# Performance work log

Hardware: AMD Instinct MI355X
Metric: run time of the kernel (lower is better)

Reference implementation:

```python
import jax, jax.numpy as jnp
import numpy as np

B, N, DIM, H, DH = 8, 1024, 512, 8, 64
INNER = H * DH
SCALE = DH ** -0.5
EPS = 1e-12  # F.normalize eps


def setup_inputs() -> dict:
    key = jax.random.key(0)
    k1, k2, k3, k4, k5 = jax.random.split(key, 5)
    x = jax.random.normal(k1, (B, N, DIM), dtype=jnp.float32)
    spd = jax.random.normal(k2, (B, 1, N, N), dtype=jnp.float32)
    # per-head binomial keep mask (one realized draw of the original loop), guaranteed nonzero
    a = np.random.RandomState(0).binomial(1, 0.9, size=H)
    if a.sum() == 0:
        a[0] = 1
    head_mask = jnp.asarray(a, dtype=jnp.float32)
    W_qkv = jax.random.normal(k3, (DIM, 3 * INNER), dtype=jnp.float32) * (DIM ** -0.5)
    W_out = jax.random.normal(k4, (INNER, DIM), dtype=jnp.float32) * (INNER ** -0.5)
    b_out = jax.random.normal(k5, (DIM,), dtype=jnp.float32) * 0.01
    return {"x": x, "spd": spd, "head_mask": head_mask,
            "W_qkv": W_qkv, "W_out": W_out, "b_out": b_out}


def reference(x, spd, head_mask, W_qkv, W_out, b_out):
    b, n, _ = x.shape
    qkv = x @ W_qkv                                   # [b, n, 3*inner]
    q, k, v = jnp.split(qkv, 3, axis=-1)
    split_heads = lambda t: t.reshape(b, n, H, DH).transpose(0, 2, 1, 3)  # b h n d
    q, k, v = split_heads(q), split_heads(k), split_heads(v)

    dots = jnp.einsum('bhnd,bhmd->bhnm', q, k) * SCALE        # [b,h,n,n]
    prod = dots * spd                                         # broadcast spd over heads
    prod_norm = jnp.sqrt(jnp.sum(prod * prod, axis=-1, keepdims=True))
    dots_norm = jnp.sqrt(jnp.sum(dots * dots, axis=-1, keepdims=True))
    bias = prod / jnp.maximum(prod_norm, EPS) * dots_norm     # F.normalize(prod)*||dots||
    attn = jax.nn.softmax(dots + bias, axis=-1)

    # head dropout mask with rescale: attn * mask * H / sum(mask)
    scale_m = head_mask * (H / jnp.sum(head_mask))
    attn = attn * scale_m[None, :, None, None]

    out = jnp.einsum('bhnm,bhmd->bhnd', attn, v)              # [b,h,n,d]
    out = out.transpose(0, 2, 1, 3).reshape(b, n, INNER)      # b n (h d)
    return out @ W_out + b_out
```

## Files before the change

### kernel.cpp

```cpp
#include <hip/hip_runtime.h>
#include <hip/hip_bf16.h>

typedef __attribute__((ext_vector_type(8))) short short8;
typedef __attribute__((ext_vector_type(4))) short s16x4;
typedef __attribute__((ext_vector_type(4))) float f32x4;

typedef const __attribute__((address_space(1))) unsigned* gp1;
typedef __attribute__((address_space(3))) unsigned* lp3;

__device__ inline short f2bf(float f) {
    union { float f; unsigned u; } v; v.f = f;
    unsigned r = v.u + 0x7fffu + ((v.u >> 16) & 1u);
    return (short)(r >> 16);
}

__global__ __launch_bounds__(256) void cvt_bf16(
    const float* __restrict__ src, short* __restrict__ dst, int n4)
{
    int i = blockIdx.x * 256 + threadIdx.x;
    if (i < n4) {
        float4 v = ((const float4*)src)[i];
        s16x4 o = { f2bf(v.x), f2bf(v.y), f2bf(v.z), f2bf(v.w) };
        ((s16x4*)dst)[i] = o;
    }
}

__global__ __launch_bounds__(256) void tr_w(
    const float* __restrict__ src, short* __restrict__ dst, int K, int N)
{
    __shared__ float t[64][65];
    const int k0 = blockIdx.x * 64, n0 = blockIdx.y * 64;
    const int r = threadIdx.x >> 4, c4 = (threadIdx.x & 15) * 4;
#pragma unroll
    for (int j = 0; j < 4; j++) {
        float4 v = *(const float4*)(src + (size_t)(k0 + r + 16 * j) * N + n0 + c4);
        t[r + 16 * j][c4 + 0] = v.x; t[r + 16 * j][c4 + 1] = v.y;
        t[r + 16 * j][c4 + 2] = v.z; t[r + 16 * j][c4 + 3] = v.w;
    }
    __syncthreads();
#pragma unroll
    for (int j = 0; j < 4; j++) {
        const int n = r + 16 * j;
        s16x4 o = { f2bf(t[c4 + 0][n]), f2bf(t[c4 + 1][n]),
                    f2bf(t[c4 + 2][n]), f2bf(t[c4 + 3][n]) };
        *(s16x4*)(dst + (size_t)(n0 + n) * K + k0 + c4) = o;
    }
}

__global__ __launch_bounds__(256) void qkv_gemm(
    const short* __restrict__ A, const short* __restrict__ BT,
    short* __restrict__ q, short* __restrict__ k, short* __restrict__ vt)
{
    __shared__ short sA[128][32];
    __shared__ short sB[64][32];

    const int tid  = threadIdx.x;
    const int wv   = tid >> 6, lane = tid & 63;
    const int quad = lane >> 4, l16 = lane & 15;
    const int m0 = blockIdx.x * 128, n0 = blockIdx.y * 64;

    f32x4 acc[2][4];
#pragma unroll
    for (int i = 0; i < 2; i++)
#pragma unroll
        for (int j = 0; j < 4; j++) acc[i][j] = (f32x4){0.f, 0.f, 0.f, 0.f};

    const short* a_src = A  + (size_t)(m0 + wv * 32 + (lane >> 2)) * 512 + (lane & 3) * 8;
    const short* b_src = BT + (size_t)(n0 + wv * 16 + (lane >> 2)) * 512 + (lane & 3) * 8;
    char* a_dst = (char*)sA + wv * 2048;
    char* b_dst = (char*)sB + wv * 1024;

    for (int ks = 0; ks < 16; ks++) {
        __syncthreads();
        const short* ap = a_src + ks * 32;
        const short* bp = b_src + ks * 32;
        __builtin_amdgcn_global_load_lds((gp1)(ap),            (lp3)(a_dst),        16, 0, 0);
        __builtin_amdgcn_global_load_lds((gp1)(ap + 16 * 512), (lp3)(a_dst + 1024), 16, 0, 0);
        __builtin_amdgcn_global_load_lds((gp1)(bp),            (lp3)(b_dst),        16, 0, 0);
        __syncthreads();

        short8 af[2], bf[4];
#pragma unroll
        for (int f = 0; f < 2; f++)
            af[f] = *(const short8*)&sA[wv * 32 + f * 16 + l16][quad * 8];
#pragma unroll
        for (int f = 0; f < 4; f++)
            bf[f] = *(const short8*)&sB[f * 16 + l16][quad * 8];
#pragma unroll
        for (int fm = 0; fm < 2; fm++)
#pragma unroll
            for (int fn = 0; fn < 4; fn++)
                acc[fm][fn] = __builtin_amdgcn_mfma_f32_16x16x32_bf16(
                    af[fm], bf[fn], acc[fm][fn], 0, 0, 0);
    }

    const int sec = n0 >> 9;
#pragma unroll
    for (int fn = 0; fn < 4; fn++) {
        const int gc = n0 + fn * 16 + l16;
        const int cc = gc & 511;
        const int h = cc >> 6, d = cc & 63;
#pragma unroll
        for (int fm = 0; fm < 2; fm++)
#pragma unroll
            for (int i = 0; i < 4; i++) {
                const int gm = m0 + wv * 32 + fm * 16 + quad * 4 + i;
                const int b = gm >> 10, n = gm & 1023;
                const int bh = b * 8 + h;
                if (sec == 0)      q[((size_t)(bh * 1024 + n)) * 64 + d] = f2bf(acc[fm][fn][i] * 0.125f);
                else if (sec == 1) k[((size_t)(bh * 1024 + n)) * 64 + d] = f2bf(acc[fm][fn][i]);
                else               vt[((size_t)(bh * 64 + d)) * 1024 + n] = f2bf(acc[fm][fn][i]);
            }
    }
}

__global__ __launch_bounds__(256, 4) void attn_k(
    const short* __restrict__ q, const short* __restrict__ kk,
    const short* __restrict__ vt, const float* __restrict__ spd,
    const float* __restrict__ hm, short* __restrict__ o)
{
    __shared__ short sK[64][72];
    __shared__ short sV[64][72];
    __shared__ short sP[4][16][72];
    __shared__ float sred[4][16];

    const int tid  = threadIdx.x;
    const int wv   = tid >> 6, lane = tid & 63;
    const int quad = lane >> 4, l16 = lane & 15;
    const int qt = blockIdx.x, bh = blockIdx.y;
    const int b = bh >> 3, h = bh & 7;
    const int q0 = qt * 64;

    const short* qb = q + ((size_t)bh * 1024 + q0 + wv * 16 + l16) * 64;
    short8 aq0 = *(const short8*)(qb + quad * 8);
    short8 aq1 = *(const short8*)(qb + 32 + quad * 8);

    const int sr = tid & 31, sc = (tid >> 5) * 8;
    const short* ksrc = kk + (size_t)bh * 65536 + (size_t)sr * 64 + sc;
    const short* vsrc = vt + (size_t)bh * 65536 + (size_t)sr * 1024 + sc;
    const float* sp   = spd + ((size_t)b * 1024 + q0 + wv * 16 + l16) * 1024 + quad * 4;

    float dn = 0.f, pn = 0.f, mxs = -1e30f, mxp = -1e30f;
    short8 k0 = *(const short8*)(ksrc);
    short8 k1 = *(const short8*)(ksrc + 2048);
    float4 sv0 = *(const float4*)(sp +  0);
    float4 sv1 = *(const float4*)(sp + 16);
    float4 sv2 = *(const float4*)(sp + 32);
    float4 sv3 = *(const float4*)(sp + 48);

    for (int c = 0; c < 16; ++c) {
        __syncthreads();
        *(short8*)&sK[sr][sc]      = k0;
        *(short8*)&sK[sr + 32][sc] = k1;
        __syncthreads();
        float4 svc0 = sv0, svc1 = sv1, svc2 = sv2, svc3 = sv3;
        if (c < 15) {
            k0 = *(const short8*)(ksrc + (c + 1) * 4096);
            k1 = *(const short8*)(ksrc + (c + 1) * 4096 + 2048);
            sv0 = *(const float4*)(sp + (c + 1) * 64 +  0);
            sv1 = *(const float4*)(sp + (c + 1) * 64 + 16);
            sv2 = *(const float4*)(sp + (c + 1) * 64 + 32);
            sv3 = *(const float4*)(sp + (c + 1) * 64 + 48);
        }
        f32x4 a[4];
#pragma unroll
        for (int t = 0; t < 4; t++) {
            a[t] = (f32x4){0.f, 0.f, 0.f, 0.f};
            a[t] = __builtin_amdgcn_mfma_f32_16x16x32_bf16(
                *(const short8*)&sK[t * 16 + l16][quad * 8], aq0, a[t], 0, 0, 0);
            a[t] = __builtin_amdgcn_mfma_f32_16x16x32_bf16(
                *(const short8*)&sK[t * 16 + l16][32 + quad * 8], aq1, a[t], 0, 0, 0);
        }
        const float4 svv[4] = {svc0, svc1, svc2, svc3};
#pragma unroll
        for (int t = 0; t < 4; t++)
#pragma unroll
            for (int i = 0; i < 4; i++) {
                float s  = a[t][i];
                float sv = ((const float*)&svv[t])[i];
                float ps = s * sv;
                dn = fmaf(s, s, dn);
                pn = fmaf(ps, ps, pn);
                mxs = fmaxf(mxs, s);
                mxp = fmaxf(mxp, ps);
            }
    }
    dn  += __shfl_xor(dn, 16, 64);  dn  += __shfl_xor(dn, 32, 64);
    pn  += __shfl_xor(pn, 16, 64);  pn  += __shfl_xor(pn, 32, 64);
    mxs = fmaxf(mxs, __shfl_xor(mxs, 16, 64)); mxs = fmaxf(mxs, __shfl_xor(mxs, 32, 64));
    mxp = fmaxf(mxp, __shfl_xor(mxp, 16, 64)); mxp = fmaxf(mxp, __shfl_xor(mxp, 32, 64));
    const float ratio = sqrtf(dn) / fmaxf(sqrtf(pn), 1e-12f);
    const float Mhat  = mxs + ratio * mxp;

    float ls = 0.f;
    f32x4 O[4];
#pragma unroll
    for (int dt = 0; dt < 4; dt++) O[dt] = (f32x4){0.f, 0.f, 0.f, 0.f};

    k0 = *(const short8*)(ksrc);
    k1 = *(const short8*)(ksrc + 2048);
    short8 v0 = *(const short8*)(vsrc);
    short8 v1 = *(const short8*)(vsrc + 32768);

    for (int c = 0; c < 16; ++c) {
        __syncthreads();
        *(short8*)&sK[sr][sc]      = k0;
        *(short8*)&sK[sr + 32][sc] = k1;
        *(short8*)&sV[sr][sc]      = v0;
        *(short8*)&sV[sr + 32][sc] = v1;
        __syncthreads();
        float4 svc0 = *(const float4*)(sp + c * 64 +  0);
        float4 svc1 = *(const float4*)(sp + c * 64 + 16);
        float4 svc2 = *(const float4*)(sp + c * 64 + 32);
        float4 svc3 = *(const float4*)(sp + c * 64 + 48);
        if (c < 15) {
            k0 = *(const short8*)(ksrc + (c + 1) * 4096);
            k1 = *(const short8*)(ksrc + (c + 1) * 4096 + 2048);
            v0 = *(const short8*)(vsrc + (c + 1) * 64);
            v1 = *(const short8*)(vsrc + (c + 1) * 64 + 32768);
        }
        f32x4 a[4];
#pragma unroll
        for (int t = 0; t < 4; t++) {
            a[t] = (f32x4){0.f, 0.f, 0.f, 0.f};
            a[t] = __builtin_amdgcn_mfma_f32_16x16x32_bf16(
                *(const short8*)&sK[t * 16 + l16][quad * 8], aq0, a[t], 0, 0, 0);
            a[t] = __builtin_amdgcn_mfma_f32_16x16x32_bf16(
                *(const short8*)&sK[t * 16 + l16][32 + quad * 8], aq1, a[t], 0, 0, 0);
        }
        const float4 svv[4] = {svc0, svc1, svc2, svc3};
#pragma unroll
        for (int t = 0; t < 4; t++) {
            float p0, p1, p2, p3;
            {
                float s = a[t][0], sv = ((const float*)&svv[t])[0];
                p0 = __expf(s * fmaf(sv, ratio, 1.0f) - Mhat);
            }
            {
                float s = a[t][1], sv = ((const float*)&svv[t])[1];
                p1 = __expf(s * fmaf(sv, ratio, 1.0f) - Mhat);
            }
            {
                float s = a[t][2], sv = ((const float*)&svv[t])[2];
                p2 = __expf(s * fmaf(sv, ratio, 1.0f) - Mhat);
            }
            {
                float s = a[t][3], sv = ((const float*)&svv[t])[3];
                p3 = __expf(s * fmaf(sv, ratio, 1.0f) - Mhat);
            }
            ls += (p0 + p1) + (p2 + p3);
            s16x4 pk = { f2bf(p0), f2bf(p1), f2bf(p2), f2bf(p3) };
            *(s16x4*)&sP[wv][l16][t * 16 + quad * 4] = pk;
        }
#pragma unroll
        for (int kc = 0; kc < 2; kc++) {
            short8 pa = *(const short8*)&sP[wv][l16][kc * 32 + quad * 8];
#pragma unroll
            for (int dt = 0; dt < 4; dt++) {
                short8 vf = *(const short8*)&sV[dt * 16 + l16][kc * 32 + quad * 8];
                O[dt] = __builtin_amdgcn_mfma_f32_16x16x32_bf16(pa, vf, O[dt], 0, 0, 0);
            }
        }
    }
    ls += __shfl_xor(ls, 16, 64); ls += __shfl_xor(ls, 32, 64);
    const float hsum = hm[0] + hm[1] + hm[2] + hm[3] + hm[4] + hm[5] + hm[6] + hm[7];
    const float rinv = hm[h] * 8.0f / (hsum * ls);
    if (quad == 0) sred[wv][l16] = rinv;
    __syncthreads();
    float rv[4];
#pragma unroll
    for (int i = 0; i < 4; i++) rv[i] = sred[wv][quad * 4 + i];
#pragma unroll
    for (int dt = 0; dt < 4; dt++)
#pragma unroll
        for (int i = 0; i < 4; i++)
            o[((size_t)(b * 1024 + q0 + wv * 16 + quad * 4 + i)) * 512 + h * 64 + dt * 16 + l16]
                = f2bf(O[dt][i] * rv[i]);
}

__global__ __launch_bounds__(256) void out_gemm(
    const short* __restrict__ A, const short* __restrict__ BT,
    const float* __restrict__ bias, float* __restrict__ out)
{
    __shared__ short sA[128][32];
    __shared__ short sB[64][32];

    const int tid  = threadIdx.x;
    const int wv   = tid >> 6, lane = tid & 63;
    const int quad = lane >> 4, l16 = lane & 15;
    const int m0 = blockIdx.x * 128, n0 = blockIdx.y * 64;

    f32x4 acc[2][4];
#pragma unroll
    for (int i = 0; i < 2; i++)
#pragma unroll
        for (int j = 0; j < 4; j++) acc[i][j] = (f32x4){0.f, 0.f, 0.f, 0.f};

    const short* a_src = A  + (size_t)(m0 + wv * 32 + (lane >> 2)) * 512 + (lane & 3) * 8;
    const short* b_src = BT + (size_t)(n0 + wv * 16 + (lane >> 2)) * 512 + (lane & 3) * 8;
    char* a_dst = (char*)sA + wv * 2048;
    char* b_dst = (char*)sB + wv * 1024;

    for (int ks = 0; ks < 16; ks++) {
        __syncthreads();
        const short* ap = a_src + ks * 32;
        const short* bp = b_src + ks * 32;
        __builtin_amdgcn_global_load_lds((gp1)(ap),            (lp3)(a_dst),        16, 0, 0);
        __builtin_amdgcn_global_load_lds((gp1)(ap + 16 * 512), (lp3)(a_dst + 1024), 16, 0, 0);
        __builtin_amdgcn_global_load_lds((gp1)(bp),            (lp3)(b_dst),        16, 0, 0);
        __syncthreads();

        short8 af[2], bf[4];
#pragma unroll
        for (int f = 0; f < 2; f++)
            af[f] = *(const short8*)&sA[wv * 32 + f * 16 + l16][quad * 8];
#pragma unroll
        for (int f = 0; f < 4; f++)
            bf[f] = *(const short8*)&sB[f * 16 + l16][quad * 8];
#pragma unroll
        for (int fm = 0; fm < 2; fm++)
#pragma unroll
            for (int fn = 0; fn < 4; fn++)
                acc[fm][fn] = __builtin_amdgcn_mfma_f32_16x16x32_bf16(
                    af[fm], bf[fn], acc[fm][fn], 0, 0, 0);
    }

#pragma unroll
    for (int fn = 0; fn < 4; fn++) {
        const int gc = n0 + fn * 16 + l16;
        const float bv = bias[gc];
#pragma unroll
        for (int fm = 0; fm < 2; fm++)
#pragma unroll
            for (int i = 0; i < 4; i++) {
                const int gm = m0 + wv * 32 + fm * 16 + quad * 4 + i;
                out[(size_t)gm * 512 + gc] = acc[fm][fn][i] + bv;
            }
    }
}

extern "C" void kernel_launch(void* const* d_in, const int* in_sizes, int n_in,
                              void* d_out, int out_size, void* d_ws, size_t ws_size,
                              hipStream_t stream) {
    const float* x    = (const float*)d_in[0];
    const float* spd  = (const float*)d_in[1];
    const float* hm   = (const float*)d_in[2];
    const float* Wqkv = (const float*)d_in[3];
    const float* Wout = (const float*)d_in[4];
    const float* bout = (const float*)d_in[5];
    float* out = (float*)d_out;

    char* ws = (char*)d_ws;
    short* qw  = (short*)(ws);
    short* kw  = (short*)(ws + ((size_t)8  << 20));
    short* vtw = (short*)(ws + ((size_t)16 << 20));
    short* ow  = (short*)(ws + ((size_t)24 << 20));
    short* xb  = (short*)(ws + ((size_t)32 << 20));
    short* wqT = (short*)(ws + ((size_t)40 << 20));
    short* woT = (short*)(ws + ((size_t)42 << 20));

    cvt_bf16<<<4096, 256, 0, stream>>>(x, xb, 8192 * 512 / 4);
    tr_w    <<<dim3(8, 24), 256, 0, stream>>>(Wqkv, wqT, 512, 1536);
    tr_w    <<<dim3(8, 8),  256, 0, stream>>>(Wout, woT, 512, 512);

    qkv_gemm<<<dim3(64, 24), 256, 0, stream>>>(xb, wqT, qw, kw, vtw);
    attn_k  <<<dim3(16, 64), 256, 0, stream>>>(qw, kw, vtw, spd, hm, ow);
    out_gemm<<<dim3(64, 8),  256, 0, stream>>>(ow, woT, bout, out);
}
```

Measured before the change: 242.7 us.

## Cache QK scores in fp16 registers across passes to skip recomputing QK^T

After: 281.7 us. 16.1% more time.

```diff
diff --git a/kernel.cpp b/kernel.cpp
--- a/kernel.cpp
+++ b/kernel.cpp
@@ -4,6 +4,7 @@
 typedef __attribute__((ext_vector_type(8))) short short8;
 typedef __attribute__((ext_vector_type(4))) short s16x4;
 typedef __attribute__((ext_vector_type(4))) float f32x4;
+typedef __attribute__((ext_vector_type(2))) _Float16 h2;
 
 typedef const __attribute__((address_space(1))) unsigned* gp1;
 typedef __attribute__((address_space(3))) unsigned* lp3;
@@ -114,7 +115,7 @@
     }
 }
 
-__global__ __launch_bounds__(256, 4) void attn_k(
+__global__ __launch_bounds__(256, 2) void attn_k(
     const short* __restrict__ q, const short* __restrict__ kk,
     const short* __restrict__ vt, const float* __restrict__ spd,
     const float* __restrict__ hm, short* __restrict__ o)
@@ -139,6 +140,8 @@
     const short* ksrc = kk + (size_t)bh * 65536 + (size_t)sr * 64 + sc;
     const short* vsrc = vt + (size_t)bh * 65536 + (size_t)sr * 1024 + sc;
     const float* sp   = spd + ((size_t)b * 1024 + q0 + wv * 16 + l16) * 1024 + quad * 4;
+
+    h2 sb[16][8];
 
     float dn = 0.f, pn = 0.f, mxs = -1e30f, mxp = -1e30f;
     short8 k0 = *(const short8*)(ksrc);
@@ -148,6 +151,7 @@
     float4 sv2 = *(const float4*)(sp + 32);
     float4 sv3 = *(const float4*)(sp + 48);
 
+#pragma unroll
     for (int c = 0; c < 16; ++c) {
         __syncthreads();
         *(short8*)&sK[sr][sc]      = k0;
@@ -173,7 +177,7 @@
         }
         const float4 svv[4] = {svc0, svc1, svc2, svc3};
 #pragma unroll
-        for (int t = 0; t < 4; t++)
+        for (int t = 0; t < 4; t++) {
 #pragma unroll
             for (int i = 0; i < 4; i++) {
                 float s  = a[t][i];
@@ -184,6 +188,9 @@
                 mxs = fmaxf(mxs, s);
                 mxp = fmaxf(mxp, ps);
             }
+            sb[c][t * 2 + 0] = (h2){(_Float16)a[t][0], (_Float16)a[t][1]};
+            sb[c][t * 2 + 1] = (h2){(_Float16)a[t][2], (_Float16)a[t][3]};
+        }
     }
     dn  += __shfl_xor(dn, 16, 64);  dn  += __shfl_xor(dn, 32, 64);
     pn  += __shfl_xor(pn, 16, 64);  pn  += __shfl_xor(pn, 32, 64);
@@ -197,15 +204,12 @@
 #pragma unroll
     for (int dt = 0; dt < 4; dt++) O[dt] = (f32x4){0.f, 0.f, 0.f, 0.f};
 
-    k0 = *(const short8*)(ksrc);
-    k1 = *(const short8*)(ksrc + 2048);
     short8 v0 = *(const short8*)(vsrc);
     short8 v1 = *(const short8*)(vsrc + 32768);
 
+#pragma unroll
     for (int c = 0; c < 16; ++c) {
         __syncthreads();
-        *(short8*)&sK[sr][sc]      = k0;
-        *(short8*)&sK[sr + 32][sc] = k1;
         *(short8*)&sV[sr][sc]      = v0;
         *(short8*)&sV[sr + 32][sc] = v1;
         __syncthreads();
@@ -214,40 +218,20 @@
         float4 svc2 = *(const float4*)(sp + c * 64 + 32);
         float4 svc3 = *(const float4*)(sp + c * 64 + 48);
         if (c < 15) {
-            k0 = *(const short8*)(ksrc + (c + 1) * 4096);
-            k1 = *(const short8*)(ksrc + (c + 1) * 4096 + 2048);
             v0 = *(const short8*)(vsrc + (c + 1) * 64);
             v1 = *(const short8*)(vsrc + (c + 1) * 64 + 32768);
         }
-        f32x4 a[4];
+        const float4 svv[4] = {svc0, svc1, svc2, svc3};
 #pragma unroll
         for (int t = 0; t < 4; t++) {
-            a[t] = (f32x4){0.f, 0.f, 0.f, 0.f};
-            a[t] = __builtin_amdgcn_mfma_f32_16x16x32_bf16(
-                *(const short8*)&sK[t * 16 + l16][quad * 8], aq0, a[t], 0, 0, 0);
-            a[t] = __builtin_amdgcn_mfma_f32_16x16x32_bf16(
-                *(const short8*)&sK[t * 16 + l16][32 + quad * 8], aq1, a[t], 0, 0, 0);
-        }
-        const float4 svv[4] = {svc0, svc1, svc2, svc3};
-#pragma unroll
-        for (int t = 0; t < 4; t++) {
-            float p0, p1, p2, p3;
-            {
-                float s = a[t][0], sv = ((const float*)&svv[t])[0];
-                p0 = __expf(s * fmaf(sv, ratio, 1.0f) - Mhat);
-            }
-            {
-                float s = a[t][1], sv = ((const float*)&svv[t])[1];
-                p1 = __expf(s * fmaf(sv, ratio, 1.0f) - Mhat);
-            }
-            {
-                float s = a[t][2], sv = ((const float*)&svv[t])[2];
-                p2 = __expf(s * fmaf(sv, ratio, 1.0f) - Mhat);
-            }
-            {
-                float s = a[t][3], sv = ((const float*)&svv[t])[3];
-                p3 = __expf(s * fmaf(sv, ratio, 1.0f) - Mhat);
-            }
+            float s0 = (float)sb[c][t * 2 + 0][0];
+            float s1 = (float)sb[c][t * 2 + 0][1];
+            float s2 = (float)sb[c][t * 2 + 1][0];
+            float s3 = (float)sb[c][t * 2 + 1][1];
+            float p0 = __expf(s0 * fmaf(((const float*)&svv[t])[0], ratio, 1.0f) - Mhat);
+            float p1 = __expf(s1 * fmaf(((const float*)&svv[t])[1], ratio, 1.0f) - Mhat);
+            float p2 = __expf(s2 * fmaf(((const float*)&svv[t])[2], ratio, 1.0f) - Mhat);
+            float p3 = __expf(s3 * fmaf(((const float*)&svv[t])[3], ratio, 1.0f) - Mhat);
             ls += (p0 + p1) + (p2 + p3);
             s16x4 pk = { f2bf(p0), f2bf(p1), f2bf(p2), f2bf(p3) };
             *(s16x4*)&sP[wv][l16][t * 16 + quad * 4] = pk;
```

## Process two 16-row query tiles per wave in attention kernel

Applied to the files above, without the earlier changes.

New measurement: 231.2 us. 1.05x faster.

```diff
diff --git a/kernel.cpp b/kernel.cpp
--- a/kernel.cpp
+++ b/kernel.cpp
@@ -114,88 +114,127 @@
     }
 }
 
-__global__ __launch_bounds__(256, 4) void attn_k(
+__global__ __launch_bounds__(256, 3) void attn_k(
     const short* __restrict__ q, const short* __restrict__ kk,
     const short* __restrict__ vt, const float* __restrict__ spd,
     const float* __restrict__ hm, short* __restrict__ o)
 {
     __shared__ short sK[64][72];
     __shared__ short sV[64][72];
-    __shared__ short sP[4][16][72];
-    __shared__ float sred[4][16];
+    __shared__ short sP[4][32][72];
+    __shared__ float sred[4][32];
 
     const int tid  = threadIdx.x;
     const int wv   = tid >> 6, lane = tid & 63;
     const int quad = lane >> 4, l16 = lane & 15;
     const int qt = blockIdx.x, bh = blockIdx.y;
     const int b = bh >> 3, h = bh & 7;
-    const int q0 = qt * 64;
-
-    const short* qb = q + ((size_t)bh * 1024 + q0 + wv * 16 + l16) * 64;
-    short8 aq0 = *(const short8*)(qb + quad * 8);
-    short8 aq1 = *(const short8*)(qb + 32 + quad * 8);
+    const int q0 = qt * 128;
+
+    const short* qbA = q + ((size_t)bh * 1024 + q0 + wv * 32 + l16) * 64;
+    short8 aqA0 = *(const short8*)(qbA + quad * 8);
+    short8 aqA1 = *(const short8*)(qbA + 32 + quad * 8);
+    const short* qbB = qbA + 16 * 64;
+    short8 aqB0 = *(const short8*)(qbB + quad * 8);
+    short8 aqB1 = *(const short8*)(qbB + 32 + quad * 8);
 
     const int sr = tid & 31, sc = (tid >> 5) * 8;
     const short* ksrc = kk + (size_t)bh * 65536 + (size_t)sr * 64 + sc;
     const short* vsrc = vt + (size_t)bh * 65536 + (size_t)sr * 1024 + sc;
-    const float* sp   = spd + ((size_t)b * 1024 + q0 + wv * 16 + l16) * 1024 + quad * 4;
-
-    float dn = 0.f, pn = 0.f, mxs = -1e30f, mxp = -1e30f;
+    const float* spA  = spd + ((size_t)b * 1024 + q0 + wv * 32 + l16) * 1024 + quad * 4;
+    const float* spB  = spA + (size_t)16 * 1024;
+
+    float dnA = 0.f, pnA = 0.f, mxsA = -1e30f, mxpA = -1e30f;
+    float dnB = 0.f, pnB = 0.f, mxsB = -1e30f, mxpB = -1e30f;
     short8 k0 = *(const short8*)(ksrc);
     short8 k1 = *(const short8*)(ksrc + 2048);
-    float4 sv0 = *(const float4*)(sp +  0);
-    float4 sv1 = *(const float4*)(sp + 16);
-    float4 sv2 = *(const float4*)(sp + 32);
-    float4 sv3 = *(const float4*)(sp + 48);
 
     for (int c = 0; c < 16; ++c) {
         __syncthreads();
         *(short8*)&sK[sr][sc]      = k0;
         *(short8*)&sK[sr + 32][sc] = k1;
         __syncthreads();
-        float4 svc0 = sv0, svc1 = sv1, svc2 = sv2, svc3 = sv3;
         if (c < 15) {
             k0 = *(const short8*)(ksrc + (c + 1) * 4096);
             k1 = *(const short8*)(ksrc + (c + 1) * 4096 + 2048);
-            sv0 = *(const float4*)(sp + (c + 1) * 64 +  0);
-            sv1 = *(const float4*)(sp + (c + 1) * 64 + 16);
-            sv2 = *(const float4*)(sp + (c + 1) * 64 + 32);
-            sv3 = *(const float4*)(sp + (c + 1) * 64 + 48);
-        }
-        f32x4 a[4];
-#pragma unroll
-        for (int t = 0; t < 4; t++) {
-            a[t] = (f32x4){0.f, 0.f, 0.f, 0.f};
-            a[t] = __builtin_amdgcn_mfma_f32_16x16x32_bf16(
-                *(const short8*)&sK[t * 16 + l16][quad * 8], aq0, a[t], 0, 0, 0);
-            a[t] = __builtin_amdgcn_mfma_f32_16x16x32_bf16(
-                *(const short8*)&sK[t * 16 + l16][32 + quad * 8], aq1, a[t], 0, 0, 0);
-        }
-        const float4 svv[4] = {svc0, svc1, svc2, svc3};
-#pragma unroll
-        for (int t = 0; t < 4; t++)
-#pragma unroll
-            for (int i = 0; i < 4; i++) {
-                float s  = a[t][i];
-                float sv = ((const float*)&svv[t])[i];
-                float ps = s * sv;
-                dn = fmaf(s, s, dn);
-                pn = fmaf(ps, ps, pn);
-                mxs = fmaxf(mxs, s);
-                mxp = fmaxf(mxp, ps);
-            }
-    }
-    dn  += __shfl_xor(dn, 16, 64);  dn  += __shfl_xor(dn, 32, 64);
-    pn  += __shfl_xor(pn, 16, 64);  pn  += __shfl_xor(pn, 32, 64);
-    mxs = fmaxf(mxs, __shfl_xor(mxs, 16, 64)); mxs = fmaxf(mxs, __shfl_xor(mxs, 32, 64));
-    mxp = fmaxf(mxp, __shfl_xor(mxp, 16, 64)); mxp = fmaxf(mxp, __shfl_xor(mxp, 32, 64));
-    const float ratio = sqrtf(dn) / fmaxf(sqrtf(pn), 1e-12f);
-    const float Mhat  = mxs + ratio * mxp;
-
-    float ls = 0.f;
-    f32x4 O[4];
-#pragma unroll
-    for (int dt = 0; dt < 4; dt++) O[dt] = (f32x4){0.f, 0.f, 0.f, 0.f};
+        }
+        {
+            float4 sv0 = *(const float4*)(spA + c * 64 +  0);
+            float4 sv1 = *(const float4*)(spA + c * 64 + 16);
+            float4 sv2 = *(const float4*)(spA + c * 64 + 32);
+            float4 sv3 = *(const float4*)(spA + c * 64 + 48);
+            f32x4 a[4];
+#pragma unroll
+            for (int t = 0; t < 4; t++) {
+                a[t] = (f32x4){0.f, 0.f, 0.f, 0.f};
+                a[t] = __builtin_amdgcn_mfma_f32_16x16x32_bf16(
+                    *(const short8*)&sK[t * 16 + l16][quad * 8], aqA0, a[t], 0, 0, 0);
+                a[t] = __builtin_amdgcn_mfma_f32_16x16x32_bf16(
+                    *(const short8*)&sK[t * 16 + l16][32 + quad * 8], aqA1, a[t], 0, 0, 0);
+            }
+            const float4 svv[4] = {sv0, sv1, sv2, sv3};
+#pragma unroll
+            for (int t = 0; t < 4; t++)
+#pragma unroll
+                for (int i = 0; i < 4; i++) {
+                    float s  = a[t][i];
+                    float sv = ((const float*)&svv[t])[i];
+                    float ps = s * sv;
+                    dnA = fmaf(s, s, dnA);
+                    pnA = fmaf(ps, ps, pnA);
+                    mxsA = fmaxf(mxsA, s);
+                    mxpA = fmaxf(mxpA, ps);
+                }
+        }
+        {
+            float4 sv0 = *(const float4*)(spB + c * 64 +  0);
+            float4 sv1 = *(const float4*)(spB + c * 64 + 16);
+            float4 sv2 = *(const float4*)(spB + c * 64 + 32);
+            float4 sv3 = *(const float4*)(spB + c * 64 + 48);
+            f32x4 a[4];
+#pragma unroll
+            for (int t = 0; t < 4; t++) {
+                a[t] = (f32x4){0.f, 0.f, 0.f, 0.f};
+                a[t] = __builtin_amdgcn_mfma_f32_16x16x32_bf16(
+                    *(const short8*)&sK[t * 16 + l16][quad * 8], aqB0, a[t], 0, 0, 0);
+                a[t] = __builtin_amdgcn_mfma_f32_16x16x32_bf16(
+                    *(const short8*)&sK[t * 16 + l16][32 + quad * 8], aqB1, a[t], 0, 0, 0);
+            }
+            const float4 svv[4] = {sv0, sv1, sv2, sv3};
+#pragma unroll
+            for (int t = 0; t < 4; t++)
+#pragma unroll
+                for (int i = 0; i < 4; i++) {
+                    float s  = a[t][i];
+                    float sv = ((const float*)&svv[t])[i];
+                    float ps = s * sv;
+                    dnB = fmaf(s, s, dnB);
+                    pnB = fmaf(ps, ps, pnB);
+                    mxsB = fmaxf(mxsB, s);
+                    mxpB = fmaxf(mxpB, ps);
+                }
+        }
+    }
+    dnA += __shfl_xor(dnA, 16, 64); dnA += __shfl_xor(dnA, 32, 64);
+    pnA += __shfl_xor(pnA, 16, 64); pnA += __shfl_xor(pnA, 32, 64);
+    dnB += __shfl_xor(dnB, 16, 64); dnB += __shfl_xor(dnB, 32, 64);
+    pnB += __shfl_xor(pnB, 16, 64); pnB += __shfl_xor(pnB, 32, 64);
+    mxsA = fmaxf(mxsA, __shfl_xor(mxsA, 16, 64)); mxsA = fmaxf(mxsA, __shfl_xor(mxsA, 32, 64));
+    mxpA = fmaxf(mxpA, __shfl_xor(mxpA, 16, 64)); mxpA = fmaxf(mxpA, __shfl_xor(mxpA, 32, 64));
+    mxsB = fmaxf(mxsB, __shfl_xor(mxsB, 16, 64)); mxsB = fmaxf(mxsB, __shfl_xor(mxsB, 32, 64));
+    mxpB = fmaxf(mxpB, __shfl_xor(mxpB, 16, 64)); mxpB = fmaxf(mxpB, __shfl_xor(mxpB, 32, 64));
+    const float ratioA = sqrtf(dnA) / fmaxf(sqrtf(pnA), 1e-12f);
+    const float ratioB = sqrtf(dnB) / fmaxf(sqrtf(pnB), 1e-12f);
+    const float MhatA  = mxsA + ratioA * mxpA;
+    const float MhatB  = mxsB + ratioB * mxpB;
+
+    float lsA = 0.f, lsB = 0.f;
+    f32x4 OA[4], OB[4];
+#pragma unroll
+    for (int dt = 0; dt < 4; dt++) {
+        OA[dt] = (f32x4){0.f, 0.f, 0.f, 0.f};
+        OB[dt] = (f32x4){0.f, 0.f, 0.f, 0.f};
+    }
 
     k0 = *(const short8*)(ksrc);
     k1 = *(const short8*)(ksrc + 2048);
@@ -209,73 +248,99 @@
         *(short8*)&sV[sr][sc]      = v0;
         *(short8*)&sV[sr + 32][sc] = v1;
         __syncthreads();
-        float4 svc0 = *(const float4*)(sp + c * 64 +  0);
-        float4 svc1 = *(const float4*)(sp + c * 64 + 16);
-        float4 svc2 = *(const float4*)(sp + c * 64 + 32);
-        float4 svc3 = *(const float4*)(sp + c * 64 + 48);
         if (c < 15) {
             k0 = *(const short8*)(ksrc + (c + 1) * 4096);
             k1 = *(const short8*)(ksrc + (c + 1) * 4096 + 2048);
             v0 = *(const short8*)(vsrc + (c + 1) * 64);
             v1 = *(const short8*)(vsrc + (c + 1) * 64 + 32768);
         }
-        f32x4 a[4];
-#pragma unroll
-        for (int t = 0; t < 4; t++) {
-            a[t] = (f32x4){0.f, 0.f, 0.f, 0.f};
-            a[t] = __builtin_amdgcn_mfma_f32_16x16x32_bf16(
-                *(const short8*)&sK[t * 16 + l16][quad * 8], aq0, a[t], 0, 0, 0);
-            a[t] = __builtin_amdgcn_mfma_f32_16x16x32_bf16(
-                *(const short8*)&sK[t * 16 + l16][32 + quad * 8], aq1, a[t], 0, 0, 0);
-        }
-        const float4 svv[4] = {svc0, svc1, svc2, svc3};
-#pragma unroll
-        for (int t = 0; t < 4; t++) {
-            float p0, p1, p2, p3;
-            {
-                float s = a[t][0], sv = ((const float*)&svv[t])[0];
-                p0 = __expf(s * fmaf(sv, ratio, 1.0f) - Mhat);
-            }
-            {
-                float s = a[t][1], sv = ((const float*)&svv[t])[1];
-                p1 = __expf(s * fmaf(sv, ratio, 1.0f) - Mhat);
-            }
-            {
-                float s = a[t][2], sv = ((const float*)&svv[t])[2];
-                p2 = __expf(s * fmaf(sv, ratio, 1.0f) - Mhat);
-            }
-            {
-                float s = a[t][3], sv = ((const float*)&svv[t])[3];
-                p3 = __expf(s * fmaf(sv, ratio, 1.0f) - Mhat);
-            }
-            ls += (p0 + p1) + (p2 + p3);
-            s16x4 pk = { f2bf(p0), f2bf(p1), f2bf(p2), f2bf(p3) };
-            *(s16x4*)&sP[wv][l16][t * 16 + quad * 4] = pk;
+        {
+            float4 sv0 = *(const float4*)(spA + c * 64 +  0);
+            float4 sv1 = *(const float4*)(spA + c * 64 + 16);
+            float4 sv2 = *(const float4*)(spA + c * 64 + 32);
+            float4 sv3 = *(const float4*)(spA + c * 64 + 48);
+            f32x4 a[4];
+#pragma unroll
+            for (int t = 0; t < 4; t++) {
+                a[t] = (f32x4){0.f, 0.f, 0.f, 0.f};
+                a[t] = __builtin_amdgcn_mfma_f32_16x16x32_bf16(
+                    *(const short8*)&sK[t * 16 + l16][quad * 8], aqA0, a[t], 0, 0, 0);
+                a[t] = __builtin_amdgcn_mfma_f32_16x16x32_bf16(
+                    *(const short8*)&sK[t * 16 + l16][32 + quad * 8], aqA1, a[t], 0, 0, 0);
+            }
+            const float4 svv[4] = {sv0, sv1, sv2, sv3};
+#pragma unroll
+            for (int t = 0; t < 4; t++) {
+                float p0 = __expf(a[t][0] * fmaf(((const float*)&svv[t])[0], ratioA, 1.0f) - MhatA);
+                float p1 = __expf(a[t][1] * fmaf(((const float*)&svv[t])[1], ratioA, 1.0f) - MhatA);
+                float p2 = __expf(a[t][2] * fmaf(((const float*)&svv[t])[2], ratioA, 1.0f) - MhatA);
+                float p3 = __expf(a[t][3] * fmaf(((const float*)&svv[t])[3], ratioA, 1.0f) - MhatA);
+                lsA += (p0 + p1) + (p2 + p3);
+                s16x4 pk = { f2bf(p0), f2bf(p1), f2bf(p2), f2bf(p3) };
+                *(s16x4*)&sP[wv][l16][t * 16 + quad * 4] = pk;
+            }
+        }
+        {
+            float4 sv0 = *(const float4*)(spB + c * 64 +  0);
+            float4 sv1 = *(const float4*)(spB + c * 64 + 16);
+            float4 sv2 = *(const float4*)(spB + c * 64 + 32);
+            float4 sv3 = *(const float4*)(spB + c * 64 + 48);
+            f32x4 a[4];
+#pragma unroll
+            for (int t = 0; t < 4; t++) {
+                a[t] = (f32x4){0.f, 0.f, 0.f, 0.f};
+                a[t] = __builtin_amdgcn_mfma_f32_16x16x32_bf16(
+                    *(const short8*)&sK[t * 16 + l16][quad * 8], aqB0, a[t], 0, 0, 0);
+                a[t] = __builtin_amdgcn_mfma_f32_16x16x32_bf16(
+                    *(const short8*)&sK[t * 16 + l16][32 + quad * 8], aqB1, a[t], 0, 0, 0);
+            }
+            const float4 svv[4] = {sv0, sv1, sv2, sv3};
+#pragma unroll
+            for (int t = 0; t < 4; t++) {
+                float p0 = __expf(a[t][0] * fmaf(((const float*)&svv[t])[0], ratioB, 1.0f) - MhatB);
+                float p1 = __expf(a[t][1] * fmaf(((const float*)&svv[t])[1], ratioB, 1.0f) - MhatB);
+                float p2 = __expf(a[t][2] * fmaf(((const float*)&svv[t])[2], ratioB, 1.0f) - MhatB);
+                float p3 = __expf(a[t][3] * fmaf(((const float*)&svv[t])[3], ratioB, 1.0f) - MhatB);
+                lsB += (p0 + p1) + (p2 + p3);
+                s16x4 pk = { f2bf(p0), f2bf(p1), f2bf(p2), f2bf(p3) };
+                *(s16x4*)&sP[wv][16 + l16][t * 16 + quad * 4] = pk;
+            }
         }
 #pragma unroll
         for (int kc = 0; kc < 2; kc++) {
-            short8 pa = *(const short8*)&sP[wv][l16][kc * 32 + quad * 8];
+            short8 paA = *(const short8*)&sP[wv][l16][kc * 32 + quad * 8];
+            short8 paB = *(const short8*)&sP[wv][16 + l16][kc * 32 + quad * 8];
 #pragma unroll
             for (int dt = 0; dt < 4; dt++) {
                 short8 vf = *(const short8*)&sV[dt * 16 + l16][kc * 32 + quad * 8];
-                O[dt] = __builtin_amdgcn_mfma_f32_16x16x32_bf16(pa, vf, O[dt], 0, 0, 0);
-            }
-        }
-    }
-    ls += __shfl_xor(ls, 16, 64); ls += __shfl_xor(ls, 32, 64);
+                OA[dt] = __builtin_amdgcn_mfma_f32_16x16x32_bf16(paA, vf, OA[dt], 0, 0, 0);
+                OB[dt] = __builtin_amdgcn_mfma_f32_16x16x32_bf16(paB, vf, OB[dt], 0, 0, 0);
+            }
+        }
+    }
+    lsA += __shfl_xor(lsA, 16, 64); lsA += __shfl_xor(lsA, 32, 64);
+    lsB += __shfl_xor(lsB, 16, 64); lsB += __shfl_xor(lsB, 32, 64);
     const float hsum = hm[0] + hm[1] + hm[2] + hm[3] + hm[4] + hm[5] + hm[6] + hm[7];
-    const float rinv = hm[h] * 8.0f / (hsum * ls);
-    if (quad == 0) sred[wv][l16] = rinv;
+    const float hscale = hm[h] * 8.0f / hsum;
+    const float rinvA = hscale / lsA;
+    const float rinvB = hscale / lsB;
+    if (quad == 0) { sred[wv][l16] = rinvA; sred[wv][16 + l16] = rinvB; }
     __syncthreads();
-    float rv[4];
-#pragma unroll
-    for (int i = 0; i < 4; i++) rv[i] = sred[wv][quad * 4 + i];
+    float rvA[4], rvB[4];
+#pragma unroll
+    for (int i = 0; i < 4; i++) {
+        rvA[i] = sred[wv][quad * 4 + i];
+        rvB[i] = sred[wv][16 + quad * 4 + i];
+    }
 #pragma unroll
     for (int dt = 0; dt < 4; dt++)
 #pragma unroll
-        for (int i = 0; i < 4; i++)
-            o[((size_t)(b * 1024 + q0 + wv * 16 + quad * 4 + i)) * 512 + h * 64 + dt * 16 + l16]
-                = f2bf(O[dt][i] * rv[i]);
+        for (int i = 0; i < 4; i++) {
+            o[((size_t)(b * 1024 + q0 + wv * 32 + quad * 4 + i)) * 512 + h * 64 + dt * 16 + l16]
+                = f2bf(OA[dt][i] * rvA[i]);
+            o[((size_t)(b * 1024 + q0 + wv * 32 + 16 + quad * 4 + i)) * 512 + h * 64 + dt * 16 + l16]
+                = f2bf(OB[dt][i] * rvB[i]);
+        }
 }
 
 __global__ __launch_bounds__(256) void out_gemm(
@@ -364,6 +429,6 @@
     tr_w    <<<dim3(8, 8),  256, 0, stream>>>(Wout, woT, 512, 512);
 
     qkv_gemm<<<dim3(64, 24), 256, 0, stream>>>(xb, wqT, qw, kw, vtw);
-    attn_k  <<<dim3(16, 64), 256, 0, stream>>>(qw, kw, vtw, spd, hm, ow);
+    attn_k  <<<dim3(8, 64),  256, 0, stream>>>(qw, kw, vtw, spd, hm, ow);
     out_gemm<<<dim3(64, 8),  256, 0, stream>>>(ow, woT, bout, out);
 }
```
